# Optimization experiments

Hardware: AMD Instinct MI355X
Metric: run time of the kernel (lower is better)

Reference implementation:

```python
import jax, jax.numpy as jnp
import numpy as np

IN_F = 2048
OUT_F = 2048
GRID = 5
BATCH = 16384

def setup_inputs() -> dict:
    key = jax.random.key(0)
    kx, kb, ks = jax.random.split(key, 3)
    x = jax.random.normal(kx, (BATCH, IN_F), dtype=jnp.float32)
    # kaiming_uniform_(a=sqrt(5)) on [out, in]: bound = sqrt(6/((1+5)*in)) = 1/sqrt(in)
    bound = 1.0 / np.sqrt(IN_F)
    base_weight = jax.random.uniform(kb, (OUT_F, IN_F), minval=-bound, maxval=bound, dtype=jnp.float32)
    spline_weights = jax.random.uniform(ks, (OUT_F, IN_F, GRID), minval=-0.1, maxval=0.1, dtype=jnp.float32)
    return {"x": x, "base_weight": base_weight, "spline_weights": spline_weights}

def reference(x, base_weight, spline_weights):
    # base path: SiLU then linear (no bias)
    base_out = jnp.einsum('bi,oi->bo', jax.nn.silu(x), base_weight)
    # RBF spline basis over fixed grid in [-1, 1]
    grid = jnp.linspace(-1.0, 1.0, GRID, dtype=x.dtype)  # [g]
    basis = jnp.exp(-((x[..., None] - grid) ** 2) * 5.0)  # [b, i, g]
    spline_out = jnp.einsum('big,oig->bo', basis, spline_weights)
    return base_out + spline_out
```

## Files before the change

### kernel.cpp

```cpp
#include <hip/hip_runtime.h>
#include <hip/hip_bf16.h>
#include <cstdint>
#include <cstddef>


#define KIN 2048
#define NOUT 2048
#define BATCH 16384
#define KEXP 12288
#define NKT 192

typedef __bf16 bf16x8 __attribute__((ext_vector_type(8)));
typedef float f32x4 __attribute__((ext_vector_type(4)));
typedef unsigned short u16x4 __attribute__((ext_vector_type(4)));

__device__ __forceinline__ unsigned short f2bf(float f) {
    union { float f; uint32_t u; } v; v.f = f;
    return (unsigned short)((v.u + 0x7FFFu + ((v.u >> 16) & 1u)) >> 16);
}

__device__ __forceinline__ void load_lds16(const void* gptr, void* lptr) {
    __builtin_amdgcn_global_load_lds(
        (const __attribute__((address_space(1))) unsigned int*)gptr,
        (__attribute__((address_space(3))) unsigned int*)lptr,
        16, 0, 0);
}

__global__ __launch_bounds__(256)
void expand_a(const float* __restrict__ X, __bf16* __restrict__ Aexp)
{
    __shared__ __align__(16) __bf16 rowbuf[KEXP];
    const int row = blockIdx.x;
    const int tid = threadIdx.x;
    const float* xrow = X + (size_t)row * KIN;

    const float K0 = 42.521082000062783f;
    const float K1 = 3.4903429574597902f;
    const float K2 = 0.2865047968601901f;
    const float K3 = 0.023517745856009107f;

    #pragma unroll
    for (int s = 0; s < 2; ++s) {
        const f32x4 xv = *(const f32x4*)(xrow + (s * 256 + tid) * 4);
        float o[24];
        #pragma unroll
        for (int e = 0; e < 4; ++e) {
            const float xf = xv[e];
            const float d0 = xf + 1.0f;
            float b = __expf(-5.0f * d0 * d0);
            const float s5 = __expf(5.0f * xf);
            o[e * 6 + 0] = b;
            b *= s5 * K0; o[e * 6 + 1] = b;
            b *= s5 * K1; o[e * 6 + 2] = b;
            b *= s5 * K2; o[e * 6 + 3] = b;
            b *= s5 * K3; o[e * 6 + 4] = b;
            o[e * 6 + 5] = xf / (1.0f + __expf(-xf));
        }
        __bf16* dst = rowbuf + (s * 1024 + tid * 4) * 6;
        #pragma unroll
        for (int q = 0; q < 3; ++q) {
            bf16x8 v;
            #pragma unroll
            for (int t = 0; t < 8; ++t) v[t] = (__bf16)o[q * 8 + t];
            *(bf16x8*)(dst + q * 8) = v;
        }
    }
    __syncthreads();
    bf16x8* out = (bf16x8*)(Aexp + (size_t)row * KEXP);
    const bf16x8* lsrc = (const bf16x8*)rowbuf;
    #pragma unroll
    for (int t = 0; t < 6; ++t)
        out[tid + t * 256] = lsrc[tid + t * 256];
}

__global__ __launch_bounds__(256)
void expand_w(const float* __restrict__ BW, const float* __restrict__ SW,
              __bf16* __restrict__ Wexp)
{
    __shared__ __align__(16) __bf16 rowbuf[KEXP];
    const int orow = blockIdx.x;
    const int tid  = threadIdx.x;

    #pragma unroll
    for (int s = 0; s < 2; ++s) {
        const int i0 = s * 1024 + tid * 4;
        const float* sb = SW + ((size_t)orow * KIN + i0) * 5;
        const f32x4 bw = *(const f32x4*)(BW + (size_t)orow * KIN + i0);
        float sw[20];
        #pragma unroll
        for (int q = 0; q < 5; ++q) {
            const f32x4 v = *(const f32x4*)(sb + q * 4);
            sw[q * 4 + 0] = v.x; sw[q * 4 + 1] = v.y;
            sw[q * 4 + 2] = v.z; sw[q * 4 + 3] = v.w;
        }
        __bf16* dst = rowbuf + (size_t)i0 * 6;
        #pragma unroll
        for (int q = 0; q < 3; ++q) {
            bf16x8 v;
            #pragma unroll
            for (int t = 0; t < 8; ++t) {
                const int e = (q * 8 + t) / 6;
                const int c = (q * 8 + t) % 6;
                v[t] = (c < 5) ? (__bf16)sw[e * 5 + c] : (__bf16)bw[e];
            }
            *(bf16x8*)(dst + q * 8) = v;
        }
    }
    __syncthreads();
    bf16x8* out = (bf16x8*)(Wexp + (size_t)orow * KEXP);
    const bf16x8* lsrc = (const bf16x8*)rowbuf;
    #pragma unroll
    for (int t = 0; t < 6; ++t)
        out[tid + t * 256] = lsrc[tid + t * 256];
}

__global__ __launch_bounds__(512, 2)
void gemm8(const __bf16* __restrict__ A, const __bf16* __restrict__ W,
           float* __restrict__ OUT)
{
    __shared__ __align__(16) __bf16 LDS[65536];
    __bf16* LA = LDS;
    __bf16* LB = LDS + 32768;

    const int tid  = threadIdx.x;
    const int lane = tid & 63;
    const int wave = tid >> 6;
    const int r    = lane & 15;
    const int quad = lane >> 4;
    const int wm   = wave >> 2;
    const int wn   = wave & 3;

    const int bid0 = blockIdx.x;
    const int bid  = (bid0 & 7) * 64 + (bid0 >> 3);
    const int mt  = bid >> 3;
    const int nt  = bid & 7;
    const int m0  = mt * 256;
    const int n0  = nt * 256;

    const int c0   = tid;
    const int c1   = tid + 512;
    const int row0 = c0 >> 2, row1 = c1 >> 2;
    const int j0   = (c0 & 3) ^ ((c0 >> 3) & 3);
    const int j1   = (c1 & 3) ^ ((c1 >> 3) & 3);
    const __bf16* srcA0 = A + (size_t)(m0 + row0) * KEXP + j0 * 8;
    const __bf16* srcA1 = A + (size_t)(m0 + row1) * KEXP + j1 * 8;
    const __bf16* srcB0 = W + (size_t)(n0 + row0) * KEXP + j0 * 8;
    const __bf16* srcB1 = W + (size_t)(n0 + row1) * KEXP + j1 * 8;

    const int dst0 = wave * 512;
    const int dst1 = 4096 + wave * 512;

    const int swz = (quad ^ ((r >> 1) & 3)) * 8;
    const __bf16* a_rd = LA + (wm * 128 + r) * 32 + swz;
    const __bf16* b_rd = LB + (wn * 64 + r) * 32 + swz;

    f32x4 acc[8][4];
    #pragma unroll
    for (int i = 0; i < 8; ++i)
        #pragma unroll
        for (int j = 0; j < 4; ++j)
            acc[i][j] = (f32x4){0.0f, 0.0f, 0.0f, 0.0f};

    bf16x8 af[4], bf[4];

#define BARX() asm volatile("s_barrier" ::: "memory")
#define VM6()  asm volatile("s_waitcnt vmcnt(6)" ::: "memory")

#define STAGE_A(buf, kh, kt) do { \
    const size_t ko = (size_t)(kt) * 64 + (kh) * 32; \
    load_lds16(srcA0 + ko, LA + ((buf) * 2 + (kh)) * 8192 + dst0); \
    load_lds16(srcA1 + ko, LA + ((buf) * 2 + (kh)) * 8192 + dst1); } while (0)

#define STAGE_B(buf, kh, kt) do { \
    const size_t ko = (size_t)(kt) * 64 + (kh) * 32; \
    load_lds16(srcB0 + ko, LB + ((buf) * 2 + (kh)) * 8192 + dst0); \
    load_lds16(srcB1 + ko, LB + ((buf) * 2 + (kh)) * 8192 + dst1); } while (0)

#define READ_A(buf, ks, a) do { \
    const __bf16* p_ = a_rd + ((buf) * 2 + (ks)) * 8192 + (a) * 2048; \
    af[0] = *(const bf16x8*)(p_); \
    af[1] = *(const bf16x8*)(p_ + 512); \
    af[2] = *(const bf16x8*)(p_ + 1024); \
    af[3] = *(const bf16x8*)(p_ + 1536); } while (0)

#define READ_B(buf, ks) do { \
    const __bf16* p_ = b_rd + ((buf) * 2 + (ks)) * 8192; \
    bf[0] = *(const bf16x8*)(p_); \
    bf[1] = *(const bf16x8*)(p_ + 512); \
    bf[2] = *(const bf16x8*)(p_ + 1024); \
    bf[3] = *(const bf16x8*)(p_ + 1536); } while (0)

#define MFMA_Q(a) do { \
    __builtin_amdgcn_s_setprio(1); \
    _Pragma("unroll") \
    for (int mi_ = 0; mi_ < 4; ++mi_) { \
        _Pragma("unroll") \
        for (int nj_ = 0; nj_ < 4; ++nj_) \
            acc[(a) * 4 + mi_][nj_] = __builtin_amdgcn_mfma_f32_16x16x32_bf16( \
                af[mi_], bf[nj_], acc[(a) * 4 + mi_][nj_], 0, 0, 0); \
    } \
    __builtin_amdgcn_s_setprio(0); } while (0)

    STAGE_B(0, 0, 0); STAGE_A(0, 0, 0); STAGE_B(0, 1, 0); STAGE_A(0, 1, 0);
    STAGE_B(1, 0, 1); STAGE_A(1, 0, 1); STAGE_B(1, 1, 1);
    VM6();
    BARX();

    for (int t = 0; t < 96; ++t) {
        const int kt1 = 2 * t + 1;
        const int sA  = (2 * t + 2 < NKT) ? 2 * t + 2 : NKT - 1;
        const int sB  = (2 * t + 3 < NKT) ? 2 * t + 3 : NKT - 1;
        READ_A(0, 0, 0); READ_B(0, 0);
        STAGE_A(1, 1, kt1);
        BARX(); MFMA_Q(0); BARX();
        READ_A(0, 0, 1);
        STAGE_B(0, 0, sA);
        BARX(); MFMA_Q(1); BARX();
        READ_A(0, 1, 1); READ_B(0, 1);
        STAGE_A(0, 0, sA);
        BARX(); MFMA_Q(1); BARX();
        READ_A(0, 1, 0);
        STAGE_B(0, 1, sA);
        VM6();
        BARX(); MFMA_Q(0); BARX();
        READ_A(1, 0, 0); READ_B(1, 0);
        STAGE_A(0, 1, sA);
        BARX(); MFMA_Q(0); BARX();
        READ_A(1, 0, 1);
        STAGE_B(1, 0, sB);
        BARX(); MFMA_Q(1); BARX();
        READ_A(1, 1, 1); READ_B(1, 1);
        STAGE_A(1, 0, sB);
        BARX(); MFMA_Q(1); BARX();
        READ_A(1, 1, 0);
        STAGE_B(1, 1, sB);
        VM6();
        BARX(); MFMA_Q(0); BARX();
    }

    #pragma unroll
    for (int fi = 0; fi < 8; ++fi) {
        #pragma unroll
        for (int nj = 0; nj < 4; ++nj) {
            const int col  = n0 + wn * 64 + nj * 16 + r;
            const int rowb = m0 + wm * 128 + fi * 16 + quad * 4;
            #pragma unroll
            for (int reg = 0; reg < 4; ++reg)
                OUT[(size_t)(rowb + reg) * NOUT + col] = acc[fi][nj][reg];
        }
    }
#undef BARX
#undef VM6
#undef STAGE_A
#undef STAGE_B
#undef READ_A
#undef READ_B
#undef MFMA_Q
}

#define BM 128
#define BN 128
#define NF 16
#define BK 96
#define LDK 104

__global__ __launch_bounds__(256)
void kan_fused(const float* __restrict__ X, const float* __restrict__ BW,
               const float* __restrict__ SW, float* __restrict__ OUT)
{
    __shared__ __align__(16) unsigned short As[BM * LDK];
    __shared__ __align__(16) unsigned short Bs[BN * LDK];

    const int tid  = threadIdx.x;
    const int lane = tid & 63;
    const int wave = tid >> 6;
    const int mt = blockIdx.x >> 4;
    const int nt = blockIdx.x & 15;
    const int m0 = mt * BM;
    const int n0 = nt * BN;
    const int r    = lane & 15;
    const int quad = lane >> 4;
    const int wm = (wave & 1) * 64;
    const int wn = (wave >> 1) * 64;

    f32x4 acc[4][4];
    #pragma unroll
    for (int i = 0; i < 4; ++i)
        #pragma unroll
        for (int j = 0; j < 4; ++j)
            acc[i][j] = (f32x4){0.0f, 0.0f, 0.0f, 0.0f};

    for (int it = 0; it < KIN / NF; ++it) {
        const int i0 = it * NF;
        __syncthreads();
        #pragma unroll
        for (int s = 0; s < 2; ++s) {
            const int slot = tid + s * 256;
            const int row  = slot >> 2;
            const int fq   = slot & 3;
            const f32x4 xv = *(const f32x4*)(X + (size_t)(m0 + row) * KIN + i0 + fq * 4);
            unsigned short basv[20];
            unsigned short silv[4];
            #pragma unroll
            for (int e = 0; e < 4; ++e) {
                const float xf = xv[e];
                silv[e] = f2bf(xf / (1.0f + __expf(-xf)));
                #pragma unroll
                for (int c = 0; c < 5; ++c) {
                    const float d = xf - (-1.0f + 0.5f * (float)c);
                    basv[e * 5 + c] = f2bf(__expf(-5.0f * d * d));
                }
            }
            unsigned short* dst = As + row * LDK + fq * 20;
            #pragma unroll
            for (int q = 0; q < 5; ++q) {
                u16x4 v;
                v.x = basv[q * 4 + 0]; v.y = basv[q * 4 + 1];
                v.z = basv[q * 4 + 2]; v.w = basv[q * 4 + 3];
                *(u16x4*)(dst + q * 4) = v;
            }
            u16x4 sv;
            sv.x = silv[0]; sv.y = silv[1]; sv.z = silv[2]; sv.w = silv[3];
            *(u16x4*)(As + row * LDK + 80 + fq * 4) = sv;
        }
        {
            const int orow = tid >> 1;
            const int half = tid & 1;
            const float* sbase = SW + (size_t)(n0 + orow) * (KIN * 5) + i0 * 5 + half * 40;
            unsigned short* brow = Bs + orow * LDK + half * 40;
            #pragma unroll
            for (int p = 0; p < 10; ++p) {
                const f32x4 wv = *(const f32x4*)(sbase + p * 4);
                u16x4 v;
                v.x = f2bf(wv.x); v.y = f2bf(wv.y);
                v.z = f2bf(wv.z); v.w = f2bf(wv.w);
                *(u16x4*)(brow + p * 4) = v;
            }
        }
        #pragma unroll
        for (int s = 0; s < 2; ++s) {
            const int slot = tid + s * 256;
            const int row  = slot >> 2;
            const int fq   = slot & 3;
            const f32x4 wv = *(const f32x4*)(BW + (size_t)(n0 + row) * KIN + i0 + fq * 4);
            u16x4 v;
            v.x = f2bf(wv.x); v.y = f2bf(wv.y);
            v.z = f2bf(wv.z); v.w = f2bf(wv.w);
            *(u16x4*)(Bs + row * LDK + 80 + fq * 4) = v;
        }
        __syncthreads();
        #pragma unroll
        for (int ks = 0; ks < 3; ++ks) {
            bf16x8 af[4], bfr[4];
            #pragma unroll
            for (int mi = 0; mi < 4; ++mi)
                af[mi] = *(const bf16x8*)(As + (wm + mi * 16 + r) * LDK + ks * 32 + quad * 8);
            #pragma unroll
            for (int ni = 0; ni < 4; ++ni)
                bfr[ni] = *(const bf16x8*)(Bs + (wn + ni * 16 + r) * LDK + ks * 32 + quad * 8);
            #pragma unroll
            for (int mi = 0; mi < 4; ++mi)
                #pragma unroll
                for (int ni = 0; ni < 4; ++ni)
                    acc[mi][ni] = __builtin_amdgcn_mfma_f32_16x16x32_bf16(
                        af[mi], bfr[ni], acc[mi][ni], 0, 0, 0);
        }
    }
    #pragma unroll
    for (int mi = 0; mi < 4; ++mi) {
        #pragma unroll
        for (int ni = 0; ni < 4; ++ni) {
            const int col  = n0 + wn + ni * 16 + r;
            const int rowb = m0 + wm + mi * 16 + quad * 4;
            #pragma unroll
            for (int reg = 0; reg < 4; ++reg)
                OUT[(size_t)(rowb + reg) * NOUT + col] = acc[mi][ni][reg];
        }
    }
}

extern "C" void kernel_launch(void* const* d_in, const int* in_sizes, int n_in,
                              void* d_out, int out_size, void* d_ws, size_t ws_size,
                              hipStream_t stream) {
    const float* X  = (const float*)d_in[0];
    const float* BW = (const float*)d_in[1];
    const float* SW = (const float*)d_in[2];
    float* OUT = (float*)d_out;

    const size_t nA = (size_t)BATCH * KEXP;
    const size_t nW = (size_t)NOUT * KEXP;
    const size_t ws_need = (nA + nW) * sizeof(__bf16);

    if (ws_size >= ws_need) {
        __bf16* Aexp = (__bf16*)d_ws;
        __bf16* Wexp = Aexp + nA;
        expand_a<<<dim3(BATCH), dim3(256), 0, stream>>>(X, Aexp);
        expand_w<<<dim3(NOUT), dim3(256), 0, stream>>>(BW, SW, Wexp);
        gemm8<<<dim3(512), dim3(512), 0, stream>>>(Aexp, Wexp, OUT);
    } else {
        kan_fused<<<dim3(128 * 16), dim3(256), 0, stream>>>(X, BW, SW, OUT);
    }
}
```

Measured before the change: 970.4 us.

## Merge expand kernels into one launch and double-buffer A fragments in GEMM loop

Combines the activation and weight expansion kernels into a single launch that picks its branch by block index, removing one launch and the tail gap between them. In the GEMM main loop, A fragments are now read into two register sets (af0/af1) so two MFMA quadrants are issued per barrier pair instead of one. This halves the barrier count per k-step and lets LDS reads for both halves go out before the MFMAs, at the cost of more VGPRs, which could hurt occupancy or cause spills under the 512x2 launch bound.

```diff
diff --git a/kernel.cpp b/kernel.cpp
--- a/kernel.cpp
+++ b/kernel.cpp
@@ -27,91 +27,87 @@
 }
 
 __global__ __launch_bounds__(256)
-void expand_a(const float* __restrict__ X, __bf16* __restrict__ Aexp)
+void expand_ab(const float* __restrict__ X, const float* __restrict__ BW,
+               const float* __restrict__ SW, __bf16* __restrict__ Aexp,
+               __bf16* __restrict__ Wexp)
 {
     __shared__ __align__(16) __bf16 rowbuf[KEXP];
-    const int row = blockIdx.x;
+    const int bid = blockIdx.x;
     const int tid = threadIdx.x;
-    const float* xrow = X + (size_t)row * KIN;
-
-    const float K0 = 42.521082000062783f;
-    const float K1 = 3.4903429574597902f;
-    const float K2 = 0.2865047968601901f;
-    const float K3 = 0.023517745856009107f;
-
-    #pragma unroll
-    for (int s = 0; s < 2; ++s) {
-        const f32x4 xv = *(const f32x4*)(xrow + (s * 256 + tid) * 4);
-        float o[24];
-        #pragma unroll
-        for (int e = 0; e < 4; ++e) {
-            const float xf = xv[e];
-            const float d0 = xf + 1.0f;
-            float b = __expf(-5.0f * d0 * d0);
-            const float s5 = __expf(5.0f * xf);
-            o[e * 6 + 0] = b;
-            b *= s5 * K0; o[e * 6 + 1] = b;
-            b *= s5 * K1; o[e * 6 + 2] = b;
-            b *= s5 * K2; o[e * 6 + 3] = b;
-            b *= s5 * K3; o[e * 6 + 4] = b;
-            o[e * 6 + 5] = xf / (1.0f + __expf(-xf));
-        }
-        __bf16* dst = rowbuf + (s * 1024 + tid * 4) * 6;
-        #pragma unroll
-        for (int q = 0; q < 3; ++q) {
-            bf16x8 v;
-            #pragma unroll
-            for (int t = 0; t < 8; ++t) v[t] = (__bf16)o[q * 8 + t];
-            *(bf16x8*)(dst + q * 8) = v;
-        }
-    }
-    __syncthreads();
-    bf16x8* out = (bf16x8*)(Aexp + (size_t)row * KEXP);
-    const bf16x8* lsrc = (const bf16x8*)rowbuf;
-    #pragma unroll
-    for (int t = 0; t < 6; ++t)
-        out[tid + t * 256] = lsrc[tid + t * 256];
-}
-
-__global__ __launch_bounds__(256)
-void expand_w(const float* __restrict__ BW, const float* __restrict__ SW,
-              __bf16* __restrict__ Wexp)
-{
-    __shared__ __align__(16) __bf16 rowbuf[KEXP];
-    const int orow = blockIdx.x;
-    const int tid  = threadIdx.x;
-
-    #pragma unroll
-    for (int s = 0; s < 2; ++s) {
-        const int i0 = s * 1024 + tid * 4;
-        const float* sb = SW + ((size_t)orow * KIN + i0) * 5;
-        const f32x4 bw = *(const f32x4*)(BW + (size_t)orow * KIN + i0);
-        float sw[20];
-        #pragma unroll
-        for (int q = 0; q < 5; ++q) {
-            const f32x4 v = *(const f32x4*)(sb + q * 4);
-            sw[q * 4 + 0] = v.x; sw[q * 4 + 1] = v.y;
-            sw[q * 4 + 2] = v.z; sw[q * 4 + 3] = v.w;
-        }
-        __bf16* dst = rowbuf + (size_t)i0 * 6;
-        #pragma unroll
-        for (int q = 0; q < 3; ++q) {
-            bf16x8 v;
-            #pragma unroll
-            for (int t = 0; t < 8; ++t) {
-                const int e = (q * 8 + t) / 6;
-                const int c = (q * 8 + t) % 6;
-                v[t] = (c < 5) ? (__bf16)sw[e * 5 + c] : (__bf16)bw[e];
-            }
-            *(bf16x8*)(dst + q * 8) = v;
-        }
-    }
-    __syncthreads();
-    bf16x8* out = (bf16x8*)(Wexp + (size_t)orow * KEXP);
-    const bf16x8* lsrc = (const bf16x8*)rowbuf;
-    #pragma unroll
-    for (int t = 0; t < 6; ++t)
-        out[tid + t * 256] = lsrc[tid + t * 256];
+
+    if (bid >= NOUT) {
+        const int row = bid - NOUT;
+        const float* xrow = X + (size_t)row * KIN;
+        const float K0 = 42.521082000062783f;
+        const float K1 = 3.4903429574597902f;
+        const float K2 = 0.2865047968601901f;
+        const float K3 = 0.023517745856009107f;
+        #pragma unroll
+        for (int s = 0; s < 2; ++s) {
+            const f32x4 xv = *(const f32x4*)(xrow + (s * 256 + tid) * 4);
+            float o[24];
+            #pragma unroll
+            for (int e = 0; e < 4; ++e) {
+                const float xf = xv[e];
+                const float d0 = xf + 1.0f;
+                float b = __expf(-5.0f * d0 * d0);
+                const float s5 = __expf(5.0f * xf);
+                o[e * 6 + 0] = b;
+                b *= s5 * K0; o[e * 6 + 1] = b;
+                b *= s5 * K1; o[e * 6 + 2] = b;
+                b *= s5 * K2; o[e * 6 + 3] = b;
+                b *= s5 * K3; o[e * 6 + 4] = b;
+                o[e * 6 + 5] = xf / (1.0f + __expf(-xf));
+            }
+            __bf16* dst = rowbuf + (s * 1024 + tid * 4) * 6;
+            #pragma unroll
+            for (int q = 0; q < 3; ++q) {
+                bf16x8 v;
+                #pragma unroll
+                for (int t = 0; t < 8; ++t) v[t] = (__bf16)o[q * 8 + t];
+                *(bf16x8*)(dst + q * 8) = v;
+            }
+        }
+        __syncthreads();
+        bf16x8* out = (bf16x8*)(Aexp + (size_t)row * KEXP);
+        const bf16x8* lsrc = (const bf16x8*)rowbuf;
+        #pragma unroll
+        for (int t = 0; t < 6; ++t)
+            out[tid + t * 256] = lsrc[tid + t * 256];
+    } else {
+        const int orow = bid;
+        #pragma unroll
+        for (int s = 0; s < 2; ++s) {
+            const int i0 = s * 1024 + tid * 4;
+            const float* sb = SW + ((size_t)orow * KIN + i0) * 5;
+            const f32x4 bw = *(const f32x4*)(BW + (size_t)orow * KIN + i0);
+            float sw[20];
+            #pragma unroll
+            for (int q = 0; q < 5; ++q) {
+                const f32x4 v = *(const f32x4*)(sb + q * 4);
+                sw[q * 4 + 0] = v.x; sw[q * 4 + 1] = v.y;
+                sw[q * 4 + 2] = v.z; sw[q * 4 + 3] = v.w;
+            }
+            __bf16* dst = rowbuf + (size_t)i0 * 6;
+            #pragma unroll
+            for (int q = 0; q < 3; ++q) {
+                bf16x8 v;
+                #pragma unroll
+                for (int t = 0; t < 8; ++t) {
+                    const int e = (q * 8 + t) / 6;
+                    const int c = (q * 8 + t) % 6;
+                    v[t] = (c < 5) ? (__bf16)sw[e * 5 + c] : (__bf16)bw[e];
+                }
+                *(bf16x8*)(dst + q * 8) = v;
+            }
+        }
+        __syncthreads();
+        bf16x8* out = (bf16x8*)(Wexp + (size_t)orow * KEXP);
+        const bf16x8* lsrc = (const bf16x8*)rowbuf;
+        #pragma unroll
+        for (int t = 0; t < 6; ++t)
+            out[tid + t * 256] = lsrc[tid + t * 256];
+    }
 }
 
 __global__ __launch_bounds__(512, 2)
@@ -161,7 +157,7 @@
         for (int j = 0; j < 4; ++j)
             acc[i][j] = (f32x4){0.0f, 0.0f, 0.0f, 0.0f};
 
-    bf16x8 af[4], bf[4];
+    bf16x8 af0[4], af1[4], bf[4];
 
 #define BARX() asm volatile("s_barrier" ::: "memory")
 #define VM6()  asm volatile("s_waitcnt vmcnt(6)" ::: "memory")
@@ -176,12 +172,12 @@
     load_lds16(srcB0 + ko, LB + ((buf) * 2 + (kh)) * 8192 + dst0); \
     load_lds16(srcB1 + ko, LB + ((buf) * 2 + (kh)) * 8192 + dst1); } while (0)
 
-#define READ_A(buf, ks, a) do { \
+#define READ_AF(arr, buf, ks, a) do { \
     const __bf16* p_ = a_rd + ((buf) * 2 + (ks)) * 8192 + (a) * 2048; \
-    af[0] = *(const bf16x8*)(p_); \
-    af[1] = *(const bf16x8*)(p_ + 512); \
-    af[2] = *(const bf16x8*)(p_ + 1024); \
-    af[3] = *(const bf16x8*)(p_ + 1536); } while (0)
+    arr[0] = *(const bf16x8*)(p_); \
+    arr[1] = *(const bf16x8*)(p_ + 512); \
+    arr[2] = *(const bf16x8*)(p_ + 1024); \
+    arr[3] = *(const bf16x8*)(p_ + 1536); } while (0)
 
 #define READ_B(buf, ks) do { \
     const __bf16* p_ = b_rd + ((buf) * 2 + (ks)) * 8192; \
@@ -190,14 +186,14 @@
     bf[2] = *(const bf16x8*)(p_ + 1024); \
     bf[3] = *(const bf16x8*)(p_ + 1536); } while (0)
 
-#define MFMA_Q(a) do { \
+#define MFMA16(frag, a) do { \
     __builtin_amdgcn_s_setprio(1); \
     _Pragma("unroll") \
     for (int mi_ = 0; mi_ < 4; ++mi_) { \
         _Pragma("unroll") \
         for (int nj_ = 0; nj_ < 4; ++nj_) \
             acc[(a) * 4 + mi_][nj_] = __builtin_amdgcn_mfma_f32_16x16x32_bf16( \
-                af[mi_], bf[nj_], acc[(a) * 4 + mi_][nj_], 0, 0, 0); \
+                frag[mi_], bf[nj_], acc[(a) * 4 + mi_][nj_], 0, 0, 0); \
     } \
     __builtin_amdgcn_s_setprio(0); } while (0)
 
@@ -210,32 +206,40 @@
         const int kt1 = 2 * t + 1;
         const int sA  = (2 * t + 2 < NKT) ? 2 * t + 2 : NKT - 1;
         const int sB  = (2 * t + 3 < NKT) ? 2 * t + 3 : NKT - 1;
-        READ_A(0, 0, 0); READ_B(0, 0);
+
+        READ_AF(af0, 0, 0, 0); READ_AF(af1, 0, 0, 1); READ_B(0, 0);
         STAGE_A(1, 1, kt1);
-        BARX(); MFMA_Q(0); BARX();
-        READ_A(0, 0, 1);
+        BARX();
+        MFMA16(af0, 0);
         STAGE_B(0, 0, sA);
-        BARX(); MFMA_Q(1); BARX();
-        READ_A(0, 1, 1); READ_B(0, 1);
+        MFMA16(af1, 1);
+        BARX();
+
+        READ_AF(af1, 0, 1, 1); READ_AF(af0, 0, 1, 0); READ_B(0, 1);
         STAGE_A(0, 0, sA);
-        BARX(); MFMA_Q(1); BARX();
-        READ_A(0, 1, 0);
+        BARX();
+        MFMA16(af1, 1);
         STAGE_B(0, 1, sA);
         VM6();
-        BARX(); MFMA_Q(0); BARX();
-        READ_A(1, 0, 0); READ_B(1, 0);
+        MFMA16(af0, 0);
+        BARX();
+
+        READ_AF(af0, 1, 0, 0); READ_AF(af1, 1, 0, 1); READ_B(1, 0);
         STAGE_A(0, 1, sA);
-        BARX(); MFMA_Q(0); BARX();
-        READ_A(1, 0, 1);
+        BARX();
+        MFMA16(af0, 0);
         STAGE_B(1, 0, sB);
-        BARX(); MFMA_Q(1); BARX();
-        READ_A(1, 1, 1); READ_B(1, 1);
+        MFMA16(af1, 1);
+        BARX();
+
+        READ_AF(af1, 1, 1, 1); READ_AF(af0, 1, 1, 0); READ_B(1, 1);
         STAGE_A(1, 0, sB);
-        BARX(); MFMA_Q(1); BARX();
-        READ_A(1, 1, 0);
+        BARX();
+        MFMA16(af1, 1);
         STAGE_B(1, 1, sB);
         VM6();
-        BARX(); MFMA_Q(0); BARX();
+        MFMA16(af0, 0);
+        BARX();
     }
 
     #pragma unroll
@@ -253,9 +257,9 @@
 #undef VM6
 #undef STAGE_A
 #undef STAGE_B
-#undef READ_A
+#undef READ_AF
 #undef READ_B
-#undef MFMA_Q
+#undef MFMA16
 }
 
 #define BM 128
@@ -394,8 +398,7 @@
     if (ws_size >= ws_need) {
         __bf16* Aexp = (__bf16*)d_ws;
         __bf16* Wexp = Aexp + nA;
-        expand_a<<<dim3(BATCH), dim3(256), 0, stream>>>(X, Aexp);
-        expand_w<<<dim3(NOUT), dim3(256), 0, stream>>>(BW, SW, Wexp);
+        expand_ab<<<dim3(NOUT + BATCH), dim3(256), 0, stream>>>(X, BW, SW, Aexp, Wexp);
         gemm8<<<dim3(512), dim3(512), 0, stream>>>(Aexp, Wexp, OUT);
     } else {
         kan_fused<<<dim3(128 * 16), dim3(256), 0, stream>>>(X, BW, SW, OUT);
```

New measurement: 973.1 us. Within noise of the previous version (+0.3%).
